# Kernel tuning notes

Measured on AMD Instinct MI355X. Metric: run time of the kernel, lower is better.

## Reference

```python
import jax, jax.numpy as jnp
import numpy as np

N = 2048          # nodes
IN_DIM = 512      # in_dim
H = 8             # num_heads
HD = IN_DIM // H  # head_dim = 64
L = 5             # max_path_len
E = 32768         # edges
D_EDGE = 64       # edge_feat_dim


def setup_inputs() -> dict:
    key = jax.random.key(0)
    ks = jax.random.split(key, 14)
    w = 1.0 / np.sqrt(IN_DIM)
    return {
        "node_feat": jax.random.normal(ks[0], (N, IN_DIM), jnp.float32),
        "edge_index": jax.random.randint(ks[1], (2, E), 0, N, dtype=jnp.int32),
        "max_path_len": 5,
        "shortest_distances": jax.random.randint(ks[2], (N, N), 0, L + 1, dtype=jnp.int32),
        "shortest_paths": jax.random.randint(ks[3], (N, N, L), 0, E + 1, dtype=jnp.int32),  # E == padding row
        "edge_feat": jax.random.normal(ks[4], (E, D_EDGE), jnp.float32),
        "attention_mask": jnp.zeros((N, N), jnp.int32),
        "WQ": jax.random.normal(ks[5], (IN_DIM, IN_DIM), jnp.float32) * w,
        "bQ": jax.random.normal(ks[6], (IN_DIM,), jnp.float32) * 0.02,
        "WK": jax.random.normal(ks[7], (IN_DIM, IN_DIM), jnp.float32) * w,
        "bK": jax.random.normal(ks[8], (IN_DIM,), jnp.float32) * 0.02,
        "WV": jax.random.normal(ks[9], (IN_DIM, IN_DIM), jnp.float32) * w,
        "bV": jax.random.normal(ks[10], (IN_DIM,), jnp.float32) * 0.02,
        "WO": jax.random.normal(ks[11], (IN_DIM, IN_DIM), jnp.float32) * w,
        "bO": jnp.zeros((IN_DIM,), jnp.float32),
        "spatial_bias": jax.random.normal(ks[12], ((L + 1) * H, 1), jnp.float32) * 0.02,
        "edge_weight": jax.random.normal(ks[13], ((L + 1) * H, D_EDGE), jnp.float32) * 0.02,
    }


def reference(node_feat, edge_index, max_path_len, shortest_distances, shortest_paths,
              edge_feat, attention_mask, WQ, bQ, WK, bK, WV, bV, WO, bO,
              spatial_bias, edge_weight):
    Nn, D = node_feat.shape
    Lp = max_path_len  # min(max_path_len, max_shortest_path_len); distances reach Lp here

    Q = (node_feat @ WQ + bQ).reshape(Nn, H, HD)
    K = (node_feat @ WK + bK).reshape(Nn, H, HD)
    V = (node_feat @ WV + bV).reshape(Nn, H, HD)

    # QK^T / sqrt(head_dim), laid out [N, N, H] as in the original after permute
    scores = jnp.einsum('nhd,mhd->nmh', Q, K) / np.sqrt(HD).astype(np.float32)

    # SpatialEncoding: bias table [(L+1)*H, 1] -> [L+1, H]; gather by clamped distance
    sp_table = spatial_bias.reshape(Lp + 1, H)
    dist = jnp.clip(shortest_distances, 0, Lp)
    scores = scores + sp_table[dist]  # [N, N, H]

    # EdgeEncoding: einsum('xyld,ldh->xyh') refactored as per-edge projection then gather
    W_e = edge_weight[: Lp * H].reshape(Lp, H, D_EDGE)  # (reshape[L,H,D].permute -> [L,D,H])
    padded = jnp.concatenate([edge_feat, jnp.zeros((1, D_EDGE), edge_feat.dtype)], axis=0)
    T = jnp.einsum('ed,lhd->elh', padded, W_e)  # [E+1, L, H]
    sp = shortest_paths[:, :, :Lp]
    gathered = T[sp, jnp.arange(Lp)[None, None, :]]  # [N, N, L, H]
    scores = scores + gathered.sum(axis=2)

    mask = attention_mask.astype(bool)
    scores = jnp.where(mask[:, :, None], -jnp.inf, scores)

    # NOTE: original applies softmax over dim=-1 of the [N, N, H] tensor (the head axis);
    # faithfully reproduced here. Dropout is identity (eval / p for inference).
    attn = jax.nn.softmax(scores, axis=-1)

    out = jnp.einsum('nmh,mhd->nhd', attn, V).reshape(Nn, D)
    return out @ WO + bO
```

## Files before the change

### kernel.cpp

```cpp
#include <hip/hip_runtime.h>

#define NN     2048
#define DIM    512
#define QKS    1024
#define NH     8
#define HD     64
#define NE     32768
#define EPAD   32832
#define CH2    8
#define LOG2E  1.4426950408889634f

typedef __attribute__((ext_vector_type(8))) short bf16x8;
typedef __attribute__((ext_vector_type(4))) float f32x4;

#define MFMA(a,b,c) __builtin_amdgcn_mfma_f32_16x16x32_bf16((a),(b),(c),0,0,0)

__device__ __forceinline__ float bf2f(unsigned int u16){
  union { unsigned int i; float f; } v; v.i = u16 << 16; return v.f;
}
__device__ __forceinline__ unsigned short f2bf(float f){
  union { float ff; unsigned int i; } v; v.ff = f;
  return (unsigned short)((v.i + 0x7fffu + ((v.i >> 16) & 1u)) >> 16);
}

__global__ __launch_bounds__(256) void cvt_k(
    const float* __restrict__ X, const float* __restrict__ ef, const float* __restrict__ ew,
    unsigned short* __restrict__ Xb, unsigned short* __restrict__ pEF, unsigned short* __restrict__ pEW)
{
  long g = (long)blockIdx.x*256 + threadIdx.x;
  const long GX = (long)NN*DIM/8;
  const long GE = (long)EPAD*8;
  const float* src; unsigned short* dst; long off, lim8;
  if (g < GX){ src = X;  dst = Xb;  off = g;        lim8 = GX; }
  else if (g < GX+GE){ src = ef; dst = pEF; off = g-GX; lim8 = (long)NE*8; }
  else { off = g-GX-GE; if (off >= 512) return; src = ew; dst = pEW; lim8 = 320; }
  unsigned short o[8];
  if (off < lim8){
    #pragma unroll
    for (int i=0;i<8;i++) o[i] = f2bf(src[off*8+i]);
  } else {
    #pragma unroll
    for (int i=0;i<8;i++) o[i] = 0;
  }
  *(uint4*)(dst + off*8) = *(const uint4*)o;
}

__global__ __launch_bounds__(256) void transpose512(
    const float* __restrict__ a0, const float* __restrict__ a1,
    const float* __restrict__ a2, const float* __restrict__ a3,
    unsigned short* __restrict__ out)
{
  __shared__ unsigned short tile[32][33];
  const float* src = blockIdx.z==0 ? a0 : blockIdx.z==1 ? a1 : blockIdx.z==2 ? a2 : a3;
  unsigned short* dst = out + (size_t)blockIdx.z*DIM*DIM;
  int bx = blockIdx.x*32, by = blockIdx.y*32;
  int tx = threadIdx.x, ty = threadIdx.y;
  #pragma unroll
  for (int i=0;i<32;i+=8) tile[ty+i][tx] = f2bf(src[(size_t)(by+ty+i)*DIM + bx+tx]);
  __syncthreads();
  #pragma unroll
  for (int i=0;i<32;i+=8) dst[(size_t)(bx+ty+i)*DIM + by+tx] = tile[tx][ty+i];
}

__global__ __launch_bounds__(256) void gemm_bt(
    const unsigned short* __restrict__ A1, const unsigned short* __restrict__ A2,
    const float* __restrict__ biasA, const float* __restrict__ biasB,
    unsigned short* __restrict__ C, float* __restrict__ Cf,
    int M, int N, int K, int bias_row)
{
  int lane = threadIdx.x & 63, w = threadIdx.x >> 6;
  int quad = lane >> 4, low = lane & 15;
  int m0 = blockIdx.y*64 + w*16;
  int n0 = blockIdx.x*64;
  f32x4 acc[4];
  #pragma unroll
  for (int t=0;t<4;t++) acc[t] = (f32x4){0.f,0.f,0.f,0.f};
  for (int k0=0; k0<K; k0+=32){
    bf16x8 a = *(const bf16x8*)(A1 + (size_t)(m0+low)*K + k0 + quad*8);
    #pragma unroll
    for (int t=0;t<4;t++){
      bf16x8 b = *(const bf16x8*)(A2 + (size_t)(n0+16*t+low)*K + k0 + quad*8);
      acc[t] = MFMA(a, b, acc[t]);
    }
  }
  #pragma unroll
  for (int t=0;t<4;t++){
    #pragma unroll
    for (int r=0;r<4;r++){
      int row = m0 + quad*4 + r;
      int col = n0 + 16*t + low;
      float v = acc[t][r];
      if (biasA){
        int bi = bias_row ? row : col;
        v += (bi < 512) ? biasA[bi] : biasB[bi-512];
      }
      if (Cf) Cf[(size_t)row*N + col] = v;
      else    C [(size_t)row*N + col] = f2bf(v);
    }
  }
}

__global__ __launch_bounds__(256) void t2_k(
    const unsigned short* __restrict__ pEF, const unsigned short* __restrict__ pEW,
    unsigned short* __restrict__ T2L)
{
  int lane = threadIdx.x & 63, w = threadIdx.x >> 6;
  int quad = lane >> 4, low = lane & 15;
  int m0 = blockIdx.y*64 + w*16;
  f32x4 acc[4];
  #pragma unroll
  for (int t=0;t<4;t++) acc[t] = (f32x4){0.f,0.f,0.f,0.f};
  #pragma unroll
  for (int k0=0; k0<64; k0+=32){
    bf16x8 a = *(const bf16x8*)(pEF + (size_t)(m0+low)*64 + k0 + quad*8);
    #pragma unroll
    for (int t=0;t<4;t++){
      bf16x8 b = *(const bf16x8*)(pEW + (size_t)(16*t+low)*64 + k0 + quad*8);
      acc[t] = MFMA(a, b, acc[t]);
    }
  }
  #pragma unroll
  for (int t=0;t<4;t++){
    #pragma unroll
    for (int r=0;r<4;r++){
      int row = m0 + quad*4 + r;
      int col = 16*t + low;
      if (col < 40)
        T2L[((size_t)(col>>3)*EPAD + row)*8 + (col&7)] = f2bf(acc[t][r]);
    }
  }
}

__global__ __launch_bounds__(256) void bias_k(
    const float* __restrict__ spb, const int* __restrict__ dist,
    const int* __restrict__ sp, const int* __restrict__ maskp,
    const unsigned short* __restrict__ T2L, unsigned short* __restrict__ biasBuf)
{
  int pix = blockIdx.x*256 + threadIdx.x;
  int dd = dist[pix];
  int msk = maskp[pix];
  const int* spp = sp + (size_t)pix*5;
  int e0 = spp[0], e1 = spp[1], e2 = spp[2], e3 = spp[3], e4 = spp[4];
  if ((unsigned)e0 > (unsigned)NE) e0 = NE;
  if ((unsigned)e1 > (unsigned)NE) e1 = NE;
  if ((unsigned)e2 > (unsigned)NE) e2 = NE;
  if ((unsigned)e3 > (unsigned)NE) e3 = NE;
  if ((unsigned)e4 > (unsigned)NE) e4 = NE;
  uint4 t0 = *(const uint4*)(T2L + ((size_t)0*EPAD + e0)*8);
  uint4 t1 = *(const uint4*)(T2L + ((size_t)1*EPAD + e1)*8);
  uint4 t2 = *(const uint4*)(T2L + ((size_t)2*EPAD + e2)*8);
  uint4 t3 = *(const uint4*)(T2L + ((size_t)3*EPAD + e3)*8);
  uint4 t4 = *(const uint4*)(T2L + ((size_t)4*EPAD + e4)*8);
  dd = dd < 0 ? 0 : (dd > 5 ? 5 : dd);
  float b[8];
  #pragma unroll
  for (int x=0;x<8;x++) b[x] = spb[dd*8 + x];
  b[0] += bf2f(t0.x & 0xffffu) + bf2f(t1.x & 0xffffu) + bf2f(t2.x & 0xffffu) + bf2f(t3.x & 0xffffu) + bf2f(t4.x & 0xffffu);
  b[1] += bf2f(t0.x >> 16)     + bf2f(t1.x >> 16)     + bf2f(t2.x >> 16)     + bf2f(t3.x >> 16)     + bf2f(t4.x >> 16);
  b[2] += bf2f(t0.y & 0xffffu) + bf2f(t1.y & 0xffffu) + bf2f(t2.y & 0xffffu) + bf2f(t3.y & 0xffffu) + bf2f(t4.y & 0xffffu);
  b[3] += bf2f(t0.y >> 16)     + bf2f(t1.y >> 16)     + bf2f(t2.y >> 16)     + bf2f(t3.y >> 16)     + bf2f(t4.y >> 16);
  b[4] += bf2f(t0.z & 0xffffu) + bf2f(t1.z & 0xffffu) + bf2f(t2.z & 0xffffu) + bf2f(t3.z & 0xffffu) + bf2f(t4.z & 0xffffu);
  b[5] += bf2f(t0.z >> 16)     + bf2f(t1.z >> 16)     + bf2f(t2.z >> 16)     + bf2f(t3.z >> 16)     + bf2f(t4.z >> 16);
  b[6] += bf2f(t0.w & 0xffffu) + bf2f(t1.w & 0xffffu) + bf2f(t2.w & 0xffffu) + bf2f(t3.w & 0xffffu) + bf2f(t4.w & 0xffffu);
  b[7] += bf2f(t0.w >> 16)     + bf2f(t1.w >> 16)     + bf2f(t2.w >> 16)     + bf2f(t3.w >> 16)     + bf2f(t4.w >> 16);
  unsigned short o[8];
  #pragma unroll
  for (int x=0;x<8;x++) o[x] = f2bf(msk ? -1e30f : b[x]);
  *(uint4*)(biasBuf + (size_t)pix*8) = *(const uint4*)o;
}

__global__ __launch_bounds__(512) void attn2_k(
    const unsigned short* __restrict__ Qb, const unsigned short* __restrict__ Kb,
    const unsigned short* __restrict__ Vt, const unsigned short* __restrict__ biasBuf,
    unsigned short* __restrict__ partO)
{
  __shared__ __attribute__((aligned(16))) unsigned short sldb[NH][16][72];
  int tid = threadIdx.x;
  int lane = tid & 63, h = tid >> 6;
  int quad = lane >> 4, low = lane & 15;
  int q0 = blockIdx.x * 16;
  int chunk = blockIdx.y;

  bf16x8 aq[2];
  #pragma unroll
  for (int s=0;s<2;s++)
    aq[s] = *(const bf16x8*)(Qb + (size_t)(q0+low)*QKS + h*HD + s*32 + quad*8);

  f32x4 accO[4];
  #pragma unroll
  for (int t=0;t<4;t++) accO[t] = (f32x4){0.f,0.f,0.f,0.f};

  uint4 bpf[2];
  #pragma unroll
  for (int it=0; it<2; ++it){
    int p = tid + it*512; int qq = p >> 6, mm = p & 63;
    bpf[it] = *(const uint4*)(biasBuf + ((size_t)(q0+qq)*NN + chunk*256 + mm)*8);
  }

  for (int jt=0; jt<4; ++jt){
    int m0 = chunk*256 + jt*64;
    __syncthreads();

    f32x4 S[4];
    #pragma unroll
    for (int t=0;t<4;t++) S[t] = (f32x4){0.f,0.f,0.f,0.f};
    #pragma unroll
    for (int s=0;s<2;s++){
      #pragma unroll
      for (int t=0;t<4;t++){
        bf16x8 bk = *(const bf16x8*)(Kb + (size_t)(m0+16*t+low)*QKS + h*HD + s*32 + quad*8);
        S[t] = MFMA(aq[s], bk, S[t]);
      }
    }
    #pragma unroll
    for (int t=0;t<4;t++){
      #pragma unroll
      for (int r=0;r<4;r++)
        sldb[h][quad*4+r][low+16*t] = f2bf(S[t][r]*0.125f);
    }
    __syncthreads();

    #pragma unroll
    for (int it=0; it<2; ++it){
      int p = tid + it*512;
      int qq = p >> 6, mm = p & 63;
      uint4 bv = bpf[it];
      if (jt < 3)
        bpf[it] = *(const uint4*)(biasBuf + ((size_t)(q0+qq)*NN + m0 + 64 + mm)*8);
      float s0[8];
      s0[0] = bf2f(sldb[0][qq][mm]) + bf2f(bv.x & 0xffffu);
      s0[1] = bf2f(sldb[1][qq][mm]) + bf2f(bv.x >> 16);
      s0[2] = bf2f(sldb[2][qq][mm]) + bf2f(bv.y & 0xffffu);
      s0[3] = bf2f(sldb[3][qq][mm]) + bf2f(bv.y >> 16);
      s0[4] = bf2f(sldb[4][qq][mm]) + bf2f(bv.z & 0xffffu);
      s0[5] = bf2f(sldb[5][qq][mm]) + bf2f(bv.z >> 16);
      s0[6] = bf2f(sldb[6][qq][mm]) + bf2f(bv.w & 0xffffu);
      s0[7] = bf2f(sldb[7][qq][mm]) + bf2f(bv.w >> 16);
      float mx = s0[0];
      #pragma unroll
      for (int x=1;x<8;x++) mx = fmaxf(mx, s0[x]);
      float sum = 0.f;
      #pragma unroll
      for (int x=0;x<8;x++){ s0[x] = exp2f((s0[x]-mx)*LOG2E); sum += s0[x]; }
      float inv = (mx < -1e29f) ? 0.f : 1.f/sum;
      #pragma unroll
      for (int x=0;x<8;x++) sldb[x][qq][mm] = f2bf(s0[x]*inv);
    }
    __syncthreads();

    #pragma unroll
    for (int s=0;s<2;s++){
      bf16x8 ap = *(const bf16x8*)&sldb[h][low][s*32 + quad*8];
      #pragma unroll
      for (int t=0;t<4;t++){
        bf16x8 bv = *(const bf16x8*)(Vt + (size_t)(h*HD + 16*t + low)*NN + m0 + s*32 + quad*8);
        accO[t] = MFMA(ap, bv, accO[t]);
      }
    }
  }

  #pragma unroll
  for (int t=0;t<4;t++){
    #pragma unroll
    for (int r=0;r<4;r++){
      int q = quad*4 + r;
      partO[((size_t)chunk*NN + q0 + q)*DIM + h*HD + 16*t + low] = f2bf(accO[t][r]);
    }
  }
}

__global__ __launch_bounds__(512) void merge_k(const unsigned short* __restrict__ pb,
                                               unsigned short* __restrict__ Obf)
{
  size_t idx = (size_t)blockIdx.x*512 + threadIdx.x;
  float s = 0.f;
  #pragma unroll
  for (int c=0;c<CH2;c++) s += bf2f(pb[(size_t)c*NN*DIM + idx]);
  Obf[idx] = f2bf(s);
}

extern "C" void kernel_launch(void* const* d_in, const int* in_sizes, int n_in,
                              void* d_out, int out_size, void* d_ws, size_t ws_size,
                              hipStream_t stream)
{
  const float* X    = (const float*)d_in[0];
  const int*  dist  = (const int*)d_in[3];
  const int*  sp    = (const int*)d_in[4];
  const float* ef   = (const float*)d_in[5];
  const int*  maskp = (const int*)d_in[6];
  const float* WQ   = (const float*)d_in[7];
  const float* bQ   = (const float*)d_in[8];
  const float* WK   = (const float*)d_in[9];
  const float* bK   = (const float*)d_in[10];
  const float* WV   = (const float*)d_in[11];
  const float* bV   = (const float*)d_in[12];
  const float* WO   = (const float*)d_in[13];
  const float* bO   = (const float*)d_in[14];
  const float* spb  = (const float*)d_in[15];
  const float* ew   = (const float*)d_in[16];

  char* ws = (char*)d_ws;
  unsigned short* Wt      = (unsigned short*)(ws + 0);
  unsigned short* Xb      = (unsigned short*)(ws + 2097152);
  unsigned short* QKb     = (unsigned short*)(ws + 4194304);
  unsigned short* Vtb     = (unsigned short*)(ws + 8388608);
  unsigned short* pEF     = (unsigned short*)(ws + 10485760);
  unsigned short* pEW     = (unsigned short*)(ws + 14688256);
  unsigned short* T2L     = (unsigned short*)(ws + 14696448);
  unsigned short* Obf     = (unsigned short*)(ws + 17323008);
  unsigned short* partO   = (unsigned short*)(ws + 19420160);
  unsigned short* biasBuf = (unsigned short*)(ws + 36197376);

  cvt_k<<<dim3(1540), dim3(256), 0, stream>>>(X, ef, ew, Xb, pEF, pEW);
  transpose512<<<dim3(16,16,4), dim3(32,8), 0, stream>>>(WQ, WK, WV, WO, Wt);
  t2_k<<<dim3(1,513), dim3(256), 0, stream>>>(pEF, pEW, T2L);
  gemm_bt<<<dim3(16,32), dim3(256), 0, stream>>>(Xb, Wt, bQ, bK, QKb, (float*)nullptr, NN, QKS, DIM, 0);
  gemm_bt<<<dim3(32,8), dim3(256), 0, stream>>>(Wt + 524288, Xb, bV, (const float*)nullptr, Vtb, (float*)nullptr, DIM, NN, DIM, 1);
  bias_k<<<dim3(16384), dim3(256), 0, stream>>>(spb, dist, sp, maskp, T2L, biasBuf);
  attn2_k<<<dim3(128,CH2), dim3(512), 0, stream>>>(QKb, QKb + 512, Vtb, biasBuf, partO);
  merge_k<<<dim3(2048), dim3(512), 0, stream>>>(partO, Obf);
  gemm_bt<<<dim3(8,32), dim3(256), 0, stream>>>(Obf, Wt + 786432, bO, (const float*)nullptr,
                                                (unsigned short*)nullptr, (float*)d_out, NN, DIM, DIM, 0);
}
```

Measured before the change: 439.5 us.

## Fuse prep kernels, compute edge table from fp32 directly, enlarge GEMM tiles

Merges the X conversion and weight transposes into one prep kernel. The edge-feature bf16 staging buffers are removed by having the edge-table MFMA kernel read fp32 and convert in registers. GEMM blocks now compute 256x64 tiles, with each wave covering a 64x64 sub-tile, which gives more A/B register reuse but launches fewer blocks. The bias gather kernel processes two pixels per thread with nontemporal loads to raise memory-level parallelism. Together these aim to cut launch count and intermediate traffic, at the cost of lower occupancy in the GEMMs.

After: 666.9 us. 51.8% more time.

```diff
diff --git a/kernel.cpp b/kernel.cpp
--- a/kernel.cpp
+++ b/kernel.cpp
@@ -12,6 +12,7 @@
 
 typedef __attribute__((ext_vector_type(8))) short bf16x8;
 typedef __attribute__((ext_vector_type(4))) float f32x4;
+typedef __attribute__((ext_vector_type(4))) unsigned int u32x4;
 
 #define MFMA(a,b,c) __builtin_amdgcn_mfma_f32_16x16x32_bf16((a),(b),(c),0,0,0)
 
@@ -22,111 +23,147 @@
   union { float ff; unsigned int i; } v; v.ff = f;
   return (unsigned short)((v.i + 0x7fffu + ((v.i >> 16) & 1u)) >> 16);
 }
-
-__global__ __launch_bounds__(256) void cvt_k(
-    const float* __restrict__ X, const float* __restrict__ ef, const float* __restrict__ ew,
-    unsigned short* __restrict__ Xb, unsigned short* __restrict__ pEF, unsigned short* __restrict__ pEW)
-{
-  long g = (long)blockIdx.x*256 + threadIdx.x;
-  const long GX = (long)NN*DIM/8;
-  const long GE = (long)EPAD*8;
-  const float* src; unsigned short* dst; long off, lim8;
-  if (g < GX){ src = X;  dst = Xb;  off = g;        lim8 = GX; }
-  else if (g < GX+GE){ src = ef; dst = pEF; off = g-GX; lim8 = (long)NE*8; }
-  else { off = g-GX-GE; if (off >= 512) return; src = ew; dst = pEW; lim8 = 320; }
-  unsigned short o[8];
-  if (off < lim8){
-    #pragma unroll
-    for (int i=0;i<8;i++) o[i] = f2bf(src[off*8+i]);
-  } else {
-    #pragma unroll
-    for (int i=0;i<8;i++) o[i] = 0;
-  }
-  *(uint4*)(dst + off*8) = *(const uint4*)o;
-}
-
-__global__ __launch_bounds__(256) void transpose512(
-    const float* __restrict__ a0, const float* __restrict__ a1,
-    const float* __restrict__ a2, const float* __restrict__ a3,
-    unsigned short* __restrict__ out)
+__device__ __forceinline__ void acc8(float* b, u32x4 v){
+  b[0] += bf2f(v[0] & 0xffffu); b[1] += bf2f(v[0] >> 16);
+  b[2] += bf2f(v[1] & 0xffffu); b[3] += bf2f(v[1] >> 16);
+  b[4] += bf2f(v[2] & 0xffffu); b[5] += bf2f(v[2] >> 16);
+  b[6] += bf2f(v[3] & 0xffffu); b[7] += bf2f(v[3] >> 16);
+}
+__device__ __forceinline__ bf16x8 pack8(float4 x0, float4 x1){
+  bf16x8 v;
+  v[0]=(short)f2bf(x0.x); v[1]=(short)f2bf(x0.y); v[2]=(short)f2bf(x0.z); v[3]=(short)f2bf(x0.w);
+  v[4]=(short)f2bf(x1.x); v[5]=(short)f2bf(x1.y); v[6]=(short)f2bf(x1.z); v[7]=(short)f2bf(x1.w);
+  return v;
+}
+
+__global__ __launch_bounds__(256) void prep_k(
+    const float* __restrict__ X,
+    const float* __restrict__ WQ, const float* __restrict__ WK,
+    const float* __restrict__ WV, const float* __restrict__ WO,
+    unsigned short* __restrict__ Xb, unsigned short* __restrict__ Wt)
 {
   __shared__ unsigned short tile[32][33];
-  const float* src = blockIdx.z==0 ? a0 : blockIdx.z==1 ? a1 : blockIdx.z==2 ? a2 : a3;
-  unsigned short* dst = out + (size_t)blockIdx.z*DIM*DIM;
-  int bx = blockIdx.x*32, by = blockIdx.y*32;
-  int tx = threadIdx.x, ty = threadIdx.y;
+  int idx = blockIdx.x, tid = threadIdx.x;
+  if (idx < 512){
+    long off = (long)idx*256 + tid;
+    const float* p = X + off*8;
+    float4 x0 = *(const float4*)p, x1 = *(const float4*)(p+4);
+    bf16x8 v = pack8(x0, x1);
+    *(bf16x8*)(Xb + off*8) = v;
+    return;
+  }
+  int b = idx - 512;
+  int z = b >> 8, t = b & 255;
+  const float* src = z==0 ? WQ : z==1 ? WK : z==2 ? WV : WO;
+  unsigned short* dst = Wt + (size_t)z*DIM*DIM;
+  int bx = (t & 15)*32, by = (t >> 4)*32;
+  int tx = tid & 31, ty = tid >> 5;
   #pragma unroll
   for (int i=0;i<32;i+=8) tile[ty+i][tx] = f2bf(src[(size_t)(by+ty+i)*DIM + bx+tx]);
   __syncthreads();
   #pragma unroll
   for (int i=0;i<32;i+=8) dst[(size_t)(bx+ty+i)*DIM + by+tx] = tile[tx][ty+i];
+}
+
+__global__ __launch_bounds__(256) void t2f_k(
+    const float* __restrict__ ef, const float* __restrict__ ew,
+    unsigned short* __restrict__ T2L)
+{
+  int lane = threadIdx.x & 63, w = threadIdx.x >> 6;
+  int quad = lane >> 4, low = lane & 15;
+  int m0 = blockIdx.x*256 + w*64;
+  f32x4 acc[4][3];
+  #pragma unroll
+  for (int im=0;im<4;im++)
+    #pragma unroll
+    for (int t=0;t<3;t++) acc[im][t] = (f32x4){0.f,0.f,0.f,0.f};
+  #pragma unroll
+  for (int k0=0;k0<64;k0+=32){
+    bf16x8 a[4], b[3];
+    #pragma unroll
+    for (int im=0;im<4;im++){
+      int e = m0 + im*16 + low;
+      bf16x8 v = (bf16x8){0,0,0,0,0,0,0,0};
+      if (e < NE){
+        const float* p = ef + (size_t)e*64 + k0 + quad*8;
+        v = pack8(*(const float4*)p, *(const float4*)(p+4));
+      }
+      a[im] = v;
+    }
+    #pragma unroll
+    for (int t=0;t<3;t++){
+      int lh = 16*t + low;
+      bf16x8 v = (bf16x8){0,0,0,0,0,0,0,0};
+      if (lh < 40){
+        const float* p = ew + (size_t)lh*64 + k0 + quad*8;
+        v = pack8(*(const float4*)p, *(const float4*)(p+4));
+      }
+      b[t] = v;
+    }
+    #pragma unroll
+    for (int im=0;im<4;im++)
+      #pragma unroll
+      for (int t=0;t<3;t++) acc[im][t] = MFMA(a[im], b[t], acc[im][t]);
+  }
+  #pragma unroll
+  for (int im=0;im<4;im++){
+    #pragma unroll
+    for (int t=0;t<3;t++){
+      #pragma unroll
+      for (int r=0;r<4;r++){
+        int row = m0 + im*16 + quad*4 + r;
+        int col = 16*t + low;
+        if (row < EPAD && col < 40)
+          T2L[((size_t)(col>>3)*EPAD + row)*8 + (col&7)] = f2bf(acc[im][t][r]);
+      }
+    }
+  }
 }
 
 __global__ __launch_bounds__(256) void gemm_bt(
     const unsigned short* __restrict__ A1, const unsigned short* __restrict__ A2,
     const float* __restrict__ biasA, const float* __restrict__ biasB,
     unsigned short* __restrict__ C, float* __restrict__ Cf,
-    int M, int N, int K, int bias_row)
+    int N, int K, int bias_row)
 {
   int lane = threadIdx.x & 63, w = threadIdx.x >> 6;
   int quad = lane >> 4, low = lane & 15;
-  int m0 = blockIdx.y*64 + w*16;
+  int m0 = blockIdx.y*256 + w*64;
   int n0 = blockIdx.x*64;
-  f32x4 acc[4];
-  #pragma unroll
-  for (int t=0;t<4;t++) acc[t] = (f32x4){0.f,0.f,0.f,0.f};
+  f32x4 acc[4][4];
+  #pragma unroll
+  for (int im=0;im<4;im++)
+    #pragma unroll
+    for (int t=0;t<4;t++) acc[im][t] = (f32x4){0.f,0.f,0.f,0.f};
   for (int k0=0; k0<K; k0+=32){
-    bf16x8 a = *(const bf16x8*)(A1 + (size_t)(m0+low)*K + k0 + quad*8);
+    bf16x8 a[4], b[4];
+    #pragma unroll
+    for (int im=0;im<4;im++)
+      a[im] = *(const bf16x8*)(A1 + (size_t)(m0+im*16+low)*K + k0 + quad*8);
+    #pragma unroll
+    for (int t=0;t<4;t++)
+      b[t] = *(const bf16x8*)(A2 + (size_t)(n0+16*t+low)*K + k0 + quad*8);
+    #pragma unroll
+    for (int im=0;im<4;im++)
+      #pragma unroll
+      for (int t=0;t<4;t++) acc[im][t] = MFMA(a[im], b[t], acc[im][t]);
+  }
+  #pragma unroll
+  for (int im=0;im<4;im++){
     #pragma unroll
     for (int t=0;t<4;t++){
-      bf16x8 b = *(const bf16x8*)(A2 + (size_t)(n0+16*t+low)*K + k0 + quad*8);
-      acc[t] = MFMA(a, b, acc[t]);
-    }
-  }
-  #pragma unroll
-  for (int t=0;t<4;t++){
-    #pragma unroll
-    for (int r=0;r<4;r++){
-      int row = m0 + quad*4 + r;
-      int col = n0 + 16*t + low;
-      float v = acc[t][r];
-      if (biasA){
-        int bi = bias_row ? row : col;
-        v += (bi < 512) ? biasA[bi] : biasB[bi-512];
-      }
-      if (Cf) Cf[(size_t)row*N + col] = v;
-      else    C [(size_t)row*N + col] = f2bf(v);
-    }
-  }
-}
-
-__global__ __launch_bounds__(256) void t2_k(
-    const unsigned short* __restrict__ pEF, const unsigned short* __restrict__ pEW,
-    unsigned short* __restrict__ T2L)
-{
-  int lane = threadIdx.x & 63, w = threadIdx.x >> 6;
-  int quad = lane >> 4, low = lane & 15;
-  int m0 = blockIdx.y*64 + w*16;
-  f32x4 acc[4];
-  #pragma unroll
-  for (int t=0;t<4;t++) acc[t] = (f32x4){0.f,0.f,0.f,0.f};
-  #pragma unroll
-  for (int k0=0; k0<64; k0+=32){
-    bf16x8 a = *(const bf16x8*)(pEF + (size_t)(m0+low)*64 + k0 + quad*8);
-    #pragma unroll
-    for (int t=0;t<4;t++){
-      bf16x8 b = *(const bf16x8*)(pEW + (size_t)(16*t+low)*64 + k0 + quad*8);
-      acc[t] = MFMA(a, b, acc[t]);
-    }
-  }
-  #pragma unroll
-  for (int t=0;t<4;t++){
-    #pragma unroll
-    for (int r=0;r<4;r++){
-      int row = m0 + quad*4 + r;
-      int col = 16*t + low;
-      if (col < 40)
-        T2L[((size_t)(col>>3)*EPAD + row)*8 + (col&7)] = f2bf(acc[t][r]);
+      #pragma unroll
+      for (int r=0;r<4;r++){
+        int row = m0 + im*16 + quad*4 + r;
+        int col = n0 + 16*t + low;
+        float v = acc[im][t][r];
+        if (biasA){
+          int bi = bias_row ? row : col;
+          v += (bi < 512) ? biasA[bi] : biasB[bi-512];
+        }
+        if (Cf) Cf[(size_t)row*N + col] = v;
+        else    C [(size_t)row*N + col] = f2bf(v);
+      }
     }
   }
 }
@@ -136,37 +173,38 @@
     const int* __restrict__ sp, const int* __restrict__ maskp,
     const unsigned short* __restrict__ T2L, unsigned short* __restrict__ biasBuf)
 {
-  int pix = blockIdx.x*256 + threadIdx.x;
-  int dd = dist[pix];
-  int msk = maskp[pix];
-  const int* spp = sp + (size_t)pix*5;
-  int e0 = spp[0], e1 = spp[1], e2 = spp[2], e3 = spp[3], e4 = spp[4];
-  if ((unsigned)e0 > (unsigned)NE) e0 = NE;
-  if ((unsigned)e1 > (unsigned)NE) e1 = NE;
-  if ((unsigned)e2 > (unsigned)NE) e2 = NE;
-  if ((unsigned)e3 > (unsigned)NE) e3 = NE;
-  if ((unsigned)e4 > (unsigned)NE) e4 = NE;
-  uint4 t0 = *(const uint4*)(T2L + ((size_t)0*EPAD + e0)*8);
-  uint4 t1 = *(const uint4*)(T2L + ((size_t)1*EPAD + e1)*8);
-  uint4 t2 = *(const uint4*)(T2L + ((size_t)2*EPAD + e2)*8);
-  uint4 t3 = *(const uint4*)(T2L + ((size_t)3*EPAD + e3)*8);
-  uint4 t4 = *(const uint4*)(T2L + ((size_t)4*EPAD + e4)*8);
-  dd = dd < 0 ? 0 : (dd > 5 ? 5 : dd);
-  float b[8];
-  #pragma unroll
-  for (int x=0;x<8;x++) b[x] = spb[dd*8 + x];
-  b[0] += bf2f(t0.x & 0xffffu) + bf2f(t1.x & 0xffffu) + bf2f(t2.x & 0xffffu) + bf2f(t3.x & 0xffffu) + bf2f(t4.x & 0xffffu);
-  b[1] += bf2f(t0.x >> 16)     + bf2f(t1.x >> 16)     + bf2f(t2.x >> 16)     + bf2f(t3.x >> 16)     + bf2f(t4.x >> 16);
-  b[2] += bf2f(t0.y & 0xffffu) + bf2f(t1.y & 0xffffu) + bf2f(t2.y & 0xffffu) + bf2f(t3.y & 0xffffu) + bf2f(t4.y & 0xffffu);
-  b[3] += bf2f(t0.y >> 16)     + bf2f(t1.y >> 16)     + bf2f(t2.y >> 16)     + bf2f(t3.y >> 16)     + bf2f(t4.y >> 16);
-  b[4] += bf2f(t0.z & 0xffffu) + bf2f(t1.z & 0xffffu) + bf2f(t2.z & 0xffffu) + bf2f(t3.z & 0xffffu) + bf2f(t4.z & 0xffffu);
-  b[5] += bf2f(t0.z >> 16)     + bf2f(t1.z >> 16)     + bf2f(t2.z >> 16)     + bf2f(t3.z >> 16)     + bf2f(t4.z >> 16);
-  b[6] += bf2f(t0.w & 0xffffu) + bf2f(t1.w & 0xffffu) + bf2f(t2.w & 0xffffu) + bf2f(t3.w & 0xffffu) + bf2f(t4.w & 0xffffu);
-  b[7] += bf2f(t0.w >> 16)     + bf2f(t1.w >> 16)     + bf2f(t2.w >> 16)     + bf2f(t3.w >> 16)     + bf2f(t4.w >> 16);
-  unsigned short o[8];
-  #pragma unroll
-  for (int x=0;x<8;x++) o[x] = f2bf(msk ? -1e30f : b[x]);
-  *(uint4*)(biasBuf + (size_t)pix*8) = *(const uint4*)o;
+  int p0 = blockIdx.x*512 + threadIdx.x;
+  int p1 = p0 + 256;
+  const int* s0 = sp + (size_t)p0*5;
+  const int* s1 = sp + (size_t)p1*5;
+  int e[10];
+  #pragma unroll
+  for (int l=0;l<5;l++){ e[l] = s0[l]; e[5+l] = s1[l]; }
+  #pragma unroll
+  for (int l=0;l<10;l++) if ((unsigned)e[l] > (unsigned)NE) e[l] = NE;
+  u32x4 t[10];
+  #pragma unroll
+  for (int l=0;l<5;l++){
+    t[l]   = __builtin_nontemporal_load((const u32x4*)(T2L + ((size_t)l*EPAD + e[l])*8));
+    t[5+l] = __builtin_nontemporal_load((const u32x4*)(T2L + ((size_t)l*EPAD + e[5+l])*8));
+  }
+  int d0 = dist[p0], d1 = dist[p1];
+  int m0 = maskp[p0], m1 = maskp[p1];
+  d0 = d0 < 0 ? 0 : (d0 > 5 ? 5 : d0);
+  d1 = d1 < 0 ? 0 : (d1 > 5 ? 5 : d1);
+  float b0[8], b1[8];
+  #pragma unroll
+  for (int x=0;x<8;x++){ b0[x] = spb[d0*8 + x]; b1[x] = spb[d1*8 + x]; }
+  #pragma unroll
+  for (int l=0;l<5;l++){ acc8(b0, t[l]); acc8(b1, t[5+l]); }
+  unsigned short o0[8], o1[8];
+  #pragma unroll
+  for (int x=0;x<8;x++){
+    o0[x] = f2bf(m0 ? -1e30f : b0[x]);
+    o1[x] = f2bf(m1 ? -1e30f : b1[x]);
+  }
+  *(uint4*)(biasBuf + (size_t)p0*8) = *(const uint4*)o0;
+  *(uint4*)(biasBuf + (size_t)p1*8) = *(const uint4*)o1;
 }
 
 __global__ __launch_bounds__(512) void attn2_k(
@@ -304,21 +342,17 @@
   unsigned short* Xb      = (unsigned short*)(ws + 2097152);
   unsigned short* QKb     = (unsigned short*)(ws + 4194304);
   unsigned short* Vtb     = (unsigned short*)(ws + 8388608);
-  unsigned short* pEF     = (unsigned short*)(ws + 10485760);
-  unsigned short* pEW     = (unsigned short*)(ws + 14688256);
-  unsigned short* T2L     = (unsigned short*)(ws + 14696448);
-  unsigned short* Obf     = (unsigned short*)(ws + 17323008);
-  unsigned short* partO   = (unsigned short*)(ws + 19420160);
-  unsigned short* biasBuf = (unsigned short*)(ws + 36197376);
-
-  cvt_k<<<dim3(1540), dim3(256), 0, stream>>>(X, ef, ew, Xb, pEF, pEW);
-  transpose512<<<dim3(16,16,4), dim3(32,8), 0, stream>>>(WQ, WK, WV, WO, Wt);
-  t2_k<<<dim3(1,513), dim3(256), 0, stream>>>(pEF, pEW, T2L);
-  gemm_bt<<<dim3(16,32), dim3(256), 0, stream>>>(Xb, Wt, bQ, bK, QKb, (float*)nullptr, NN, QKS, DIM, 0);
-  gemm_bt<<<dim3(32,8), dim3(256), 0, stream>>>(Wt + 524288, Xb, bV, (const float*)nullptr, Vtb, (float*)nullptr, DIM, NN, DIM, 1);
-  bias_k<<<dim3(16384), dim3(256), 0, stream>>>(spb, dist, sp, maskp, T2L, biasBuf);
+  unsigned short* T2L     = (unsigned short*)(ws + 10485760);
+  unsigned short* Obf     = (unsigned short*)(ws + 13112320);
+  unsigned short* partO   = (unsigned short*)(ws + 15209472);
+  unsigned short* biasBuf = (unsigned short*)(ws + 31986688);
+
+  prep_k<<<dim3(1536), dim3(256), 0, stream>>>(X, WQ, WK, WV, WO, Xb, Wt);
+  t2f_k<<<dim3(129), dim3(256), 0, stream>>>(ef, ew, T2L);
+  gemm_bt<<<dim3(16,8), dim3(256), 0, stream>>>(Xb, Wt, bQ, bK, QKb, (float*)nullptr, QKS, DIM, 0);
+  gemm_bt<<<dim3(32,2), dim3(256), 0, stream>>>(Wt + 524288, Xb, bV, (const float*)nullptr, Vtb, (float*)nullptr, NN, DIM, 1);
+  bias_k<<<dim3(8192), dim3(256), 0, stream>>>(spb, dist, sp, maskp, T2L, biasBuf);
   attn2_k<<<dim3(128,CH2), dim3(512), 0, stream>>>(QKb, QKb + 512, Vtb, biasBuf, partO);
   merge_k<<<dim3(2048), dim3(512), 0, stream>>>(partO, Obf);
-  gemm_bt<<<dim3(8,32), dim3(256), 0, stream>>>(Obf, Wt + 786432, bO, (const float*)nullptr,
-                                                (unsigned short*)nullptr, (float*)d_out, NN, DIM, DIM, 0);
-}
+  gemm_bt<<<dim3(8,8), dim3(256), 0, stream>>>(Obf, Wt + 786432, bO, bO, (unsigned short*)nullptr, (float*)d_out, DIM, DIM, 0);
+}
```
